# Optimization experiments

Hardware: AMD Instinct MI355X
Metric: run time of the kernel (lower is better)

## Reference

```python
import jax, jax.numpy as jnp
import numpy as np

D_MODEL = 2048
N_HEADS = 16
N_KV = 4
GROUP = N_HEADS // N_KV  # 4
D_K = D_MODEL // N_HEADS  # 128
D_V = D_MODEL // N_KV     # 512
THETA = 10000.0
Q_DIM = N_HEADS * D_K
K_DIM = N_KV * D_K
V_DIM = N_KV * D_V


def _apply_rope(t, sin, cos):
    # t: [B, H, L, D]; sin/cos: [L, D] broadcast over batch/heads
    half = t.shape[-1] // 2
    x1, x2 = t[..., :half], t[..., half:]
    rot = jnp.concatenate([-x2, x1], axis=-1)
    return t * cos + rot * sin


def setup_inputs() -> dict:
    key = jax.random.key(0)
    k1, k2, k3 = jax.random.split(key, 3)
    x = jax.random.normal(k1, (2, 2048, D_MODEL), dtype=jnp.float32)
    # attn_proj: Linear(d_model -> Q_DIM+K_DIM+V_DIM, bias=False); stored as [in, out]
    W_attn = jax.random.normal(k2, (D_MODEL, Q_DIM + K_DIM + V_DIM), dtype=jnp.float32) * 0.02
    # out_proj: Linear(n_heads*d_v -> d_model) with bias
    W_out = jax.random.normal(k3, (N_HEADS * D_V, D_MODEL), dtype=jnp.float32) * 0.02
    b_out = jnp.zeros((D_MODEL,), dtype=jnp.float32)
    return {"x": x, "W_attn": W_attn, "W_out": W_out, "b_out": b_out}


def reference(x, W_attn, W_out, b_out):
    B, L, _ = x.shape
    qkv = x @ W_attn  # [B, L, Q_DIM+K_DIM+V_DIM]
    q = qkv[..., :Q_DIM].reshape(B, L, N_HEADS, D_K).transpose(0, 2, 1, 3)          # [B,H,L,dk]
    k = qkv[..., Q_DIM:Q_DIM + K_DIM].reshape(B, L, N_KV, D_K).transpose(0, 2, 1, 3)  # [B,Hkv,L,dk]
    v = qkv[..., Q_DIM + K_DIM:].reshape(B, L, N_KV, D_V).transpose(0, 2, 1, 3)       # [B,Hkv,L,dv]

    # RoPE (computed in float32, as in source)
    inv_freq = 1.0 / (THETA ** (jnp.arange(0, D_K, 2, dtype=jnp.float32) / D_K))
    freqs = jnp.arange(L, dtype=jnp.float32)[:, None] * inv_freq[None, :]  # [L, dk/2]
    ang = jnp.concatenate([freqs, freqs], axis=-1)                          # [L, dk]
    sin, cos = jnp.sin(ang), jnp.cos(ang)
    q = _apply_rope(q.astype(jnp.float32), sin, cos).astype(x.dtype)
    k = _apply_rope(k.astype(jnp.float32), sin, cos).astype(x.dtype)

    # GQA: repeat_interleave(group, dim=1) is equivalent to grouping q heads as [kv, group]
    qg = q.reshape(B, N_KV, GROUP, L, D_K)
    scores = jnp.einsum('bkgqd,bkld->bkgql', qg, k) / (D_K ** 0.5)  # [B,Hkv,G,L,L]
    probs = jax.nn.softmax(scores, axis=-1)
    ctx = jnp.einsum('bkgql,bkle->bkgqe', probs, v)  # [B,Hkv,G,L,dv]
    ctx = ctx.reshape(B, N_HEADS, L, D_V).transpose(0, 2, 1, 3).reshape(B, L, N_HEADS * D_V)
    return ctx @ W_out + b_out
```

## Files before the change

kernel.cpp:

```cpp
#include <hip/hip_runtime.h>

typedef unsigned short u16;
typedef float f32x4 __attribute__((ext_vector_type(4)));
typedef __bf16 bf16x8 __attribute__((ext_vector_type(8)));

#define DEV static __device__ __forceinline__

DEV u16 f2bf(float f) {
  union { float f; unsigned u; } c; c.f = f;
  unsigned u = c.u;
  u += 0x7fffu + ((u >> 16) & 1u);
  return (u16)(u >> 16);
}
DEV float bf2f(u16 h) {
  union { float f; unsigned u; } c; c.u = ((unsigned)h) << 16;
  return c.f;
}
DEV f32x4 MFMA(bf16x8 a, bf16x8 b, f32x4 c) {
  return __builtin_amdgcn_mfma_f32_16x16x32_bf16(a, b, c, 0, 0, 0);
}
DEV unsigned cvt_pk_bf16(float a, float b) {
  unsigned r;
  asm("v_cvt_pk_bf16_f32 %0, %1, %2" : "=v"(r) : "v"(a), "v"(b));
  return r;
}
DEV float ex2(float x) { return __builtin_amdgcn_exp2f(x); }
DEV void glds16(const void* src, void* lds) {
  __builtin_amdgcn_global_load_lds(
      (__attribute__((address_space(1))) void*)src,
      (__attribute__((address_space(3))) void*)lds, 16, 0, 0);
}
DEV void barrier_raw() {
  __builtin_amdgcn_sched_barrier(0);
  asm volatile("s_barrier" ::: "memory");
  __builtin_amdgcn_sched_barrier(0);
}
#define VMCNT(N)                                              \
  do {                                                        \
    asm volatile("s_waitcnt vmcnt(" #N ")" ::: "memory");     \
    __builtin_amdgcn_sched_barrier(0);                        \
  } while (0)


__global__ void rope_tables(float* __restrict__ sinT, float* __restrict__ cosT) {
  int idx = blockIdx.x * 256 + threadIdx.x;
  int l = idx >> 6, i = idx & 63;
  float inv = __expf(-((float)(2 * i) / 128.0f) * 9.210340371976184f);
  float ang = (float)l * inv;
  sinT[idx] = sinf(ang);
  cosT[idx] = cosf(ang);
}

__global__ void cast_f32_bf16(const float* __restrict__ in, u16* __restrict__ out) {
  int i = (blockIdx.x * 256 + threadIdx.x) * 4;
  float4 v = *(const float4*)(in + i);
  ushort4 o;
  o.x = f2bf(v.x); o.y = f2bf(v.y); o.z = f2bf(v.z); o.w = f2bf(v.w);
  *(ushort4*)(out + i) = o;
}

__global__ void transpose_cast(const float* __restrict__ in, u16* __restrict__ out,
                               int R, int C) {
  __shared__ u16 tile[32][33];
  int c0 = blockIdx.x * 32, r0 = blockIdx.y * 32;
  int tx = threadIdx.x, ty = threadIdx.y;
  for (int i = 0; i < 32; i += 8)
    tile[ty + i][tx] = f2bf(in[(size_t)(r0 + ty + i) * C + c0 + tx]);
  __syncthreads();
  for (int i = 0; i < 32; i += 8)
    out[(size_t)(c0 + ty + i) * R + r0 + tx] = tile[tx][ty + i];
}

__global__ __launch_bounds__(512) void gemm1_8ph(const u16* __restrict__ A,
                                                 const u16* __restrict__ Bt,
                                                 u16* __restrict__ C) {
  constexpr int K = 2048, N = 4608, NT = 32;
  __shared__ __align__(16) u16 lA[2][2][8192];
  __shared__ __align__(16) u16 lB[2][2][8192];
  const int t = threadIdx.x, w = t >> 6, l = t & 63;
  const int lr = l & 15, lg = l >> 4;
  const int wr = w >> 2, wn = w & 3;
  const int swz = (blockIdx.x & 7) * 36 + (blockIdx.x >> 3);
  const int bm = swz & 15, bn = swz >> 4;

  const size_t aBase = (size_t)(bm * 256) * K;
  const size_t bBase = (size_t)(bn * 256) * K;
  const int lslog = (t & 3) ^ ((t >> 3) & 3);
  const int r128 = t >> 2;
  const int aswz = (lg ^ ((lr >> 1) & 3)) << 4;

  auto stA = [&](int buf, int kk, int tile) {
#pragma unroll
    for (int i = 0; i < 2; ++i) {
      int row = i * 128 + r128;
      glds16(A + aBase + (size_t)row * K + tile * 64 + kk * 32 + lslog * 8,
             &lA[buf][kk][i * 4096 + t * 8]);
    }
  };
  auto stB = [&](int buf, int kk, int tile) {
#pragma unroll
    for (int i = 0; i < 2; ++i) {
      int row = i * 128 + r128;
      glds16(Bt + bBase + (size_t)row * K + tile * 64 + kk * 32 + lslog * 8,
             &lB[buf][kk][i * 4096 + t * 8]);
    }
  };

  f32x4 acc[8][4];
#pragma unroll
  for (int f = 0; f < 8; ++f)
#pragma unroll
    for (int g = 0; g < 4; ++g) acc[f][g] = f32x4{0.f, 0.f, 0.f, 0.f};

  stA(0, 0, 0); stB(0, 0, 0); stA(0, 1, 0); stB(0, 1, 0); stA(1, 0, 1); stB(1, 0, 1);
  VMCNT(8);
  barrier_raw();

  auto PH = [&](int buf, int kk, int mh, auto&& st) {
    bf16x8 af[4], bb[4];
    const char* pA = (const char*)lA[buf][kk];
    const char* pB = (const char*)lB[buf][kk];
#pragma unroll
    for (int f = 0; f < 4; ++f) {
      af[f] = *(const bf16x8*)(pA + (wr * 128 + (mh * 4 + f) * 16 + lr) * 64 + aswz);
      bb[f] = *(const bf16x8*)(pB + (wn * 64 + f * 16 + lr) * 64 + aswz);
    }
    st();
    __builtin_amdgcn_s_setprio(1);
#pragma unroll
    for (int f = 0; f < 4; ++f)
#pragma unroll
      for (int g = 0; g < 4; ++g)
        acc[mh * 4 + f][g] = MFMA(af[f], bb[g], acc[mh * 4 + f][g]);
    __builtin_amdgcn_s_setprio(0);
  };
  auto NOST = [] {};

  for (int i = 0; i < NT / 2 - 1; ++i) {
    const int t1 = 2 * i + 1, t2 = 2 * i + 2, t3 = 2 * i + 3;
    PH(0, 0, 0, [&] { stA(1, 1, t1); });            barrier_raw();
    PH(0, 0, 1, [&] { stB(1, 1, t1); }); VMCNT(8);  barrier_raw();
    PH(0, 1, 0, [&] { stA(0, 0, t2); });            barrier_raw();
    PH(0, 1, 1, [&] { stB(0, 0, t2); }); VMCNT(8);  barrier_raw();
    PH(1, 0, 0, [&] { stA(0, 1, t2); });            barrier_raw();
    PH(1, 0, 1, [&] { stB(0, 1, t2); }); VMCNT(8);  barrier_raw();
    PH(1, 1, 0, [&] { stA(1, 0, t3); });            barrier_raw();
    PH(1, 1, 1, [&] { stB(1, 0, t3); }); VMCNT(8);  barrier_raw();
  }
  PH(0, 0, 0, [&] { stA(1, 1, NT - 1); });           barrier_raw();
  PH(0, 0, 1, [&] { stB(1, 1, NT - 1); }); VMCNT(8); barrier_raw();
  PH(0, 1, 0, NOST);                                 barrier_raw();
  PH(0, 1, 1, NOST);                       VMCNT(4); barrier_raw();
  PH(1, 0, 0, NOST);                                 barrier_raw();
  PH(1, 0, 1, NOST);                       VMCNT(0); barrier_raw();
  PH(1, 1, 0, NOST);                                 barrier_raw();
  PH(1, 1, 1, NOST);

  const int crow0 = bm * 256 + wr * 128;
  const int ccol0 = bn * 256 + wn * 64;
#pragma unroll
  for (int f = 0; f < 8; ++f)
#pragma unroll
    for (int g = 0; g < 4; ++g)
#pragma unroll
      for (int j = 0; j < 4; ++j)
        C[(size_t)(crow0 + f * 16 + lg * 4 + j) * N + ccol0 + g * 16 + lr] =
            f2bf(acc[f][g][j]);
}

__global__ __launch_bounds__(512) void gemm2_4ph(const u16* __restrict__ A,
                                                 const u16* __restrict__ Bt,
                                                 float* __restrict__ Cf,
                                                 const float* __restrict__ bias) {
  constexpr int K = 8192, N = 2048, NT = 128;
  __shared__ __align__(16) u16 lA[2][2][8192];
  __shared__ __align__(16) u16 lB[2][2][4096];
  const int t = threadIdx.x, w = t >> 6, l = t & 63;
  const int lr = l & 15, lg = l >> 4;
  const int wr = w >> 1, wn = w & 1;
  const int swz = (blockIdx.x & 7) * 32 + (blockIdx.x >> 3);
  const int bm = swz & 15, bn = swz >> 4;

  const size_t aBase = (size_t)(bm * 256) * K;
  const size_t bBase = (size_t)(bn * 128) * K;
  const int lslog = (t & 3) ^ ((t >> 3) & 3);
  const int r128 = t >> 2;
  const int aswz = (lg ^ ((lr >> 1) & 3)) << 4;

  auto stA = [&](int buf, int kk, int tile) {
#pragma unroll
    for (int i = 0; i < 2; ++i) {
      int row = i * 128 + r128;
      glds16(A + aBase + (size_t)row * K + tile * 64 + kk * 32 + lslog * 8,
             &lA[buf][kk][i * 4096 + t * 8]);
    }
  };
  auto stB = [&](int buf, int kk, int tile) {
    glds16(Bt + bBase + (size_t)r128 * K + tile * 64 + kk * 32 + lslog * 8,
           &lB[buf][kk][t * 8]);
  };

  f32x4 acc[4][4];
#pragma unroll
  for (int f = 0; f < 4; ++f)
#pragma unroll
    for (int g = 0; g < 4; ++g) acc[f][g] = f32x4{0.f, 0.f, 0.f, 0.f};

  stA(0, 0, 0); stB(0, 0, 0); stA(0, 1, 0); stB(0, 1, 0); stA(1, 0, 1); stB(1, 0, 1);
  VMCNT(6);
  barrier_raw();

  auto PH = [&](int buf, int kk, auto&& st) {
    bf16x8 af[4], bb[4];
    const char* pA = (const char*)lA[buf][kk];
    const char* pB = (const char*)lB[buf][kk];
#pragma unroll
    for (int f = 0; f < 4; ++f) {
      af[f] = *(const bf16x8*)(pA + (wr * 64 + f * 16 + lr) * 64 + aswz);
      bb[f] = *(const bf16x8*)(pB + (wn * 64 + f * 16 + lr) * 64 + aswz);
    }
    st();
    __builtin_amdgcn_s_setprio(1);
#pragma unroll
    for (int f = 0; f < 4; ++f)
#pragma unroll
      for (int g = 0; g < 4; ++g)
        acc[f][g] = MFMA(af[f], bb[g], acc[f][g]);
    __builtin_amdgcn_s_setprio(0);
  };
  auto NOST = [] {};

  for (int i = 0; i < NT / 2 - 1; ++i) {
    const int t1 = 2 * i + 1, t2 = 2 * i + 2, t3 = 2 * i + 3;
    PH(0, 0, [&] { stA(1, 1, t1); stB(1, 1, t1); }); VMCNT(6); barrier_raw();
    PH(0, 1, [&] { stA(0, 0, t2); stB(0, 0, t2); }); VMCNT(6); barrier_raw();
    PH(1, 0, [&] { stA(0, 1, t2); stB(0, 1, t2); }); VMCNT(6); barrier_raw();
    PH(1, 1, [&] { stA(1, 0, t3); stB(1, 0, t3); }); VMCNT(6); barrier_raw();
  }
  PH(0, 0, [&] { stA(1, 1, NT - 1); stB(1, 1, NT - 1); }); VMCNT(6); barrier_raw();
  PH(0, 1, NOST);                                          VMCNT(3); barrier_raw();
  PH(1, 0, NOST);                                          VMCNT(0); barrier_raw();
  PH(1, 1, NOST);

  const int crow0 = bm * 256 + wr * 64;
  const int ccol0 = bn * 128 + wn * 64;
#pragma unroll
  for (int g = 0; g < 4; ++g) {
    float bv = bias[ccol0 + g * 16 + lr];
#pragma unroll
    for (int f = 0; f < 4; ++f)
#pragma unroll
      for (int j = 0; j < 4; ++j)
        Cf[(size_t)(crow0 + f * 16 + lg * 4 + j) * N + ccol0 + g * 16 + lr] =
            acc[f][g][j] + bv;
  }
}

__global__ void rope_kernel(u16* __restrict__ qkv, const float* __restrict__ sinT,
                            const float* __restrict__ cosT) {
  int idx = blockIdx.x * 256 + threadIdx.x;
  int d = idx & 63;
  int rh = idx >> 6;
  int head = rh % 20;
  int row = rh / 20;
  int lpos = row & 2047;
  int col = head < 16 ? head * 128 : 2048 + (head - 16) * 128;
  float sc = head < 16 ? 0.12751743561938476f : 1.0f;
  u16* p = qkv + (size_t)row * 4608 + col;
  float x1 = bf2f(p[d]), x2 = bf2f(p[d + 64]);
  float c = cosT[lpos * 64 + d], s = sinT[lpos * 64 + d];
  p[d]      = f2bf((x1 * c - x2 * s) * sc);
  p[d + 64] = f2bf((x2 * c + x1 * s) * sc);
}

__global__ void vt_kernel(const u16* __restrict__ qkv, u16* __restrict__ vT) {
  __shared__ u16 tile[32][33];
  int bkv = blockIdx.z;
  int b = bkv >> 2, kv = bkv & 3;
  int e0 = blockIdx.x * 32, l0 = blockIdx.y * 32;
  const u16* src = qkv + (size_t)(b * 2048) * 4608 + 2560 + kv * 512;
  int tx = threadIdx.x, ty = threadIdx.y;
  for (int i = 0; i < 32; i += 8)
    tile[ty + i][tx] = src[(size_t)(l0 + ty + i) * 4608 + e0 + tx];
  __syncthreads();
  u16* dst = vT + (size_t)(bkv * 512) * 2048;
  int pi = ((tx >> 2) & 3) * 8 + ((tx >> 4) & 1) * 4 + (tx & 3);
  for (int i = 0; i < 32; i += 8)
    dst[(size_t)(e0 + ty + i) * 2048 + l0 + pi] = tile[tx][ty + i];
}

__global__ __launch_bounds__(512, 2) void attn_kernel(
    const u16* __restrict__ qkv, const u16* __restrict__ vT,
    u16* __restrict__ ctxb) {
  const int wg = blockIdx.x;
  const int pg = wg & 7, qt = wg >> 3;
  const int kvg = pg & 3, b = pg >> 2;
  const int t = threadIdx.x, w = t >> 6, l = t & 63;
  const int lr = l & 15, lg = l >> 4;
  const int h4 = w >> 1, eh = w & 1;
  const int h = kvg * 4 + h4;

  __shared__ __align__(16) u16 lK[2][32 * 128];
  __shared__ __align__(16) u16 lV[2][256 * 64];

  f32x4 zero = {0.f, 0.f, 0.f, 0.f};

  bf16x8 qf[2][4];
  const size_t qbase = (size_t)(b * 2048 + qt * 32);
#pragma unroll
  for (int m = 0; m < 2; ++m)
#pragma unroll
    for (int dc = 0; dc < 4; ++dc)
      qf[m][dc] = *(const bf16x8*)(qkv + (qbase + m * 16 + lr) * 4608 + h * 128 + dc * 32 + lg * 8);

  f32x4 acc[2][16];
#pragma unroll
  for (int m = 0; m < 2; ++m)
#pragma unroll
    for (int e = 0; e < 16; ++e) acc[m][e] = zero;
  float m_r[2] = {-1e30f, -1e30f};
  float l_r[2] = {0.f, 0.f};

  const size_t kbase = (size_t)(b * 2048) * 4608 + 2048 + kvg * 128;
  const size_t vbase = (size_t)((b * 4 + kvg) * 512) * 2048;

  const int krow = t >> 4;
  const int kp = t & 15;
  const int ks = (kp & 8) | ((kp ^ (krow & 7)) & 7);
  const u16* ksrc0 = qkv + kbase + (size_t)krow * 4608 + ks * 8;
  const int vs = (t & 7) ^ ((t >> 3) & 7);
  const int ve0 = (t >> 3) * 2 + (vs >> 2);
  const u16* vsrc0 = vT + vbase + (size_t)ve0 * 2048 + (vs & 3) * 8;

  const int vfoff = (eh * 128 + (lr >> 1)) * 128 +
                    (((((lr & 1) << 2) | lg) ^ ((lr >> 1) & 7)) << 4);

  auto stage = [&](int bi, int kv0) {
    glds16(ksrc0 + (size_t)kv0 * 4608, &lK[bi][t * 8]);
#pragma unroll
    for (int i = 0; i < 4; ++i)
      glds16(vsrc0 + kv0 + (size_t)i * 262144, &lV[bi][i * 4096 + t * 8]);
  };

  stage(0, 0);

  for (int it = 0; it < 64; ++it) {
    const int cur = it & 1;
    __syncthreads();
    if (it + 1 < 64) stage(cur ^ 1, 32 * (it + 1));
    const char* lKc = (const char*)lK[cur];
    const char* lVc = (const char*)lV[cur];

    f32x4 sT[2][2];
    sT[0][0] = zero; sT[0][1] = zero; sT[1][0] = zero; sT[1][1] = zero;
#pragma unroll
    for (int dc = 0; dc < 4; ++dc) {
      int slot = dc * 4 + lg;
      int sw = (slot & 8) | ((slot ^ (lr & 7)) & 7);
#pragma unroll
      for (int kt = 0; kt < 2; ++kt) {
        bf16x8 kf = *(const bf16x8*)(lKc + (kt * 16 + lr) * 256 + sw * 16);
        sT[kt][0] = MFMA(kf, qf[0][dc], sT[kt][0]);
        sT[kt][1] = MFMA(kf, qf[1][dc], sT[kt][1]);
      }
    }

    float rmax[2];
#pragma unroll
    for (int m = 0; m < 2; ++m) {
      float a0 = fmaxf(fmaxf(sT[0][m][0], sT[0][m][1]), fmaxf(sT[0][m][2], sT[0][m][3]));
      float a1 = fmaxf(fmaxf(sT[1][m][0], sT[1][m][1]), fmaxf(sT[1][m][2], sT[1][m][3]));
      float r = fmaxf(a0, a1);
      r = fmaxf(r, __shfl_xor(r, 16));
      r = fmaxf(r, __shfl_xor(r, 32));
      rmax[m] = r;
    }
    bool need = (rmax[0] > m_r[0] + 11.5f) || (rmax[1] > m_r[1] + 11.5f);
    if (__any(need)) {
#pragma unroll
      for (int m = 0; m < 2; ++m) {
        float mn = fmaxf(m_r[m], rmax[m]);
        float al = ex2(m_r[m] - mn);
        m_r[m] = mn; l_r[m] *= al;
        float alj[4];
#pragma unroll
        for (int j = 0; j < 4; ++j) alj[j] = __shfl(al, lg * 4 + j);
#pragma unroll
        for (int e = 0; e < 16; ++e)
#pragma unroll
          for (int j = 0; j < 4; ++j) acc[m][e][j] *= alj[j];
      }
    }

    bf16x8 pf[2];
#pragma unroll
    for (int m = 0; m < 2; ++m) {
      float p0 = ex2(sT[0][m][0] - m_r[m]), p1 = ex2(sT[0][m][1] - m_r[m]);
      float p2 = ex2(sT[0][m][2] - m_r[m]), p3 = ex2(sT[0][m][3] - m_r[m]);
      float p4 = ex2(sT[1][m][0] - m_r[m]), p5 = ex2(sT[1][m][1] - m_r[m]);
      float p6 = ex2(sT[1][m][2] - m_r[m]), p7 = ex2(sT[1][m][3] - m_r[m]);
      float s = ((p0 + p1) + (p2 + p3)) + ((p4 + p5) + (p6 + p7));
      s += __shfl_xor(s, 16);
      s += __shfl_xor(s, 32);
      l_r[m] += s;
      union { bf16x8 v; unsigned wd[4]; } u;
      u.wd[0] = cvt_pk_bf16(p0, p1);
      u.wd[1] = cvt_pk_bf16(p2, p3);
      u.wd[2] = cvt_pk_bf16(p4, p5);
      u.wd[3] = cvt_pk_bf16(p6, p7);
      pf[m] = u.v;
    }

#pragma unroll
    for (int e = 0; e < 16; ++e) {
      bf16x8 vf = *(const bf16x8*)(lVc + vfoff + e * 1024);
      acc[0][e] = MFMA(pf[0], vf, acc[0][e]);
      acc[1][e] = MFMA(pf[1], vf, acc[1][e]);
    }
  }

#pragma unroll
  for (int m = 0; m < 2; ++m) {
    float linv[4];
#pragma unroll
    for (int j = 0; j < 4; ++j) linv[j] = 1.0f / __shfl(l_r[m], lg * 4 + j);
    const size_t orow0 = qbase + m * 16 + lg * 4;
#pragma unroll
    for (int e = 0; e < 16; ++e)
#pragma unroll
      for (int j = 0; j < 4; ++j)
        ctxb[(orow0 + j) * 8192 + h * 512 + eh * 256 + e * 16 + lr] =
            f2bf(acc[m][e][j] * linv[j]);
  }
}

extern "C" void kernel_launch(void* const* d_in, const int* in_sizes, int n_in,
                              void* d_out, int out_size, void* d_ws, size_t ws_size,
                              hipStream_t stream) {
  const float* x      = (const float*)d_in[0];
  const float* W_attn = (const float*)d_in[1];
  const float* W_out  = (const float*)d_in[2];
  const float* b_out  = (const float*)d_in[3];
  float* out = (float*)d_out;
  char* ws = (char*)d_ws;

  if (ws_size < 158334976u) return;

  float* sinT = (float*)(ws + 0);
  float* cosT = (float*)(ws + 524288);
  u16* xb   = (u16*)(ws + 1048576);
  u16* WbT  = (u16*)(ws + 17825792);
  u16* qkvb = (u16*)(ws + 36700160);
  u16* vT   = (u16*)(ws + 74448896);
  u16* ctxb = (u16*)(ws + 91226112);
  u16* WobT = (u16*)(ws + 1048576);

  rope_tables<<<512, 256, 0, stream>>>(sinT, cosT);
  cast_f32_bf16<<<8192, 256, 0, stream>>>(x, xb);
  transpose_cast<<<dim3(144, 64), dim3(32, 8), 0, stream>>>(W_attn, WbT, 2048, 4608);
  gemm1_8ph<<<288, 512, 0, stream>>>(xb, WbT, qkvb);
  rope_kernel<<<20480, 256, 0, stream>>>(qkvb, sinT, cosT);
  vt_kernel<<<dim3(16, 64, 8), dim3(32, 8), 0, stream>>>(qkvb, vT);
  attn_kernel<<<512, 512, 0, stream>>>(qkvb, vT, ctxb);
  transpose_cast<<<dim3(64, 256), dim3(32, 8), 0, stream>>>(W_out, WobT, 8192, 2048);
  gemm2_4ph<<<256, 512, 0, stream>>>(ctxb, WobT, out, b_out);
}
```

Baseline: 571.6 us.

## Software-pipeline PV matmul one iteration behind QK with triple-buffered V

Restructures the attention loop so the P·V MFMAs for the previous tile run interleaved with the exp computations of the current tile, using a triple-buffered V LDS ring so the previous tile's V stays resident. When a max-rescale is needed, the pending PV is flushed before rescaling. It also adds s_setprio around the MFMA sections. The aim is to overlap transcendental/VALU work with matrix work. In exchange, LDS use grows by one 32 KB V buffer, which may reduce occupancy below 2 workgroups per CU, and register pressure rises.

```diff
diff --git a/kernel.cpp b/kernel.cpp
--- a/kernel.cpp
+++ b/kernel.cpp
@@ -301,7 +301,7 @@
   const int h = kvg * 4 + h4;
 
   __shared__ __align__(16) u16 lK[2][32 * 128];
-  __shared__ __align__(16) u16 lV[2][256 * 64];
+  __shared__ __align__(16) u16 lV[3][256 * 64];
 
   f32x4 zero = {0.f, 0.f, 0.f, 0.f};
 
@@ -335,24 +335,32 @@
   const int vfoff = (eh * 128 + (lr >> 1)) * 128 +
                     (((((lr & 1) << 2) | lg) ^ ((lr >> 1) & 7)) << 4);
 
-  auto stage = [&](int bi, int kv0) {
-    glds16(ksrc0 + (size_t)kv0 * 4608, &lK[bi][t * 8]);
+  auto stageK = [&](int kb, int kv0) {
+    glds16(ksrc0 + (size_t)kv0 * 4608, &lK[kb][t * 8]);
+  };
+  auto stageV = [&](u16* vbuf, int kv0) {
 #pragma unroll
     for (int i = 0; i < 4; ++i)
-      glds16(vsrc0 + kv0 + (size_t)i * 262144, &lV[bi][i * 4096 + t * 8]);
-  };
-
-  stage(0, 0);
+      glds16(vsrc0 + kv0 + (size_t)i * 262144, vbuf + i * 4096 + t * 8);
+  };
+
+  u16* vP = lV[2];
+  u16* vC = lV[0];
+  u16* vS = lV[1];
+
+  stageK(0, 0); stageV(vC, 0);
+
+  bf16x8 pfp[2];
 
   for (int it = 0; it < 64; ++it) {
-    const int cur = it & 1;
     __syncthreads();
-    if (it + 1 < 64) stage(cur ^ 1, 32 * (it + 1));
-    const char* lKc = (const char*)lK[cur];
-    const char* lVc = (const char*)lV[cur];
+    if (it + 1 < 64) { stageK((it + 1) & 1, 32 * (it + 1)); stageV(vS, 32 * (it + 1)); }
+    const char* lKc = (const char*)lK[it & 1];
+    const char* vPc = (const char*)vP;
 
     f32x4 sT[2][2];
     sT[0][0] = zero; sT[0][1] = zero; sT[1][0] = zero; sT[1][1] = zero;
+    __builtin_amdgcn_s_setprio(1);
 #pragma unroll
     for (int dc = 0; dc < 4; ++dc) {
       int slot = dc * 4 + lg;
@@ -364,6 +372,20 @@
         sT[kt][1] = MFMA(kf, qf[1][dc], sT[kt][1]);
       }
     }
+    __builtin_amdgcn_s_setprio(0);
+
+    auto PVC = [&](int c) {
+      if (it) {
+        __builtin_amdgcn_s_setprio(1);
+#pragma unroll
+        for (int e = c * 4; e < c * 4 + 4; ++e) {
+          bf16x8 vf = *(const bf16x8*)(vPc + vfoff + e * 1024);
+          acc[0][e] = MFMA(pfp[0], vf, acc[0][e]);
+          acc[1][e] = MFMA(pfp[1], vf, acc[1][e]);
+        }
+        __builtin_amdgcn_s_setprio(0);
+      }
+    };
 
     float rmax[2];
 #pragma unroll
@@ -376,7 +398,9 @@
       rmax[m] = r;
     }
     bool need = (rmax[0] > m_r[0] + 11.5f) || (rmax[1] > m_r[1] + 11.5f);
+
     if (__any(need)) {
+      PVC(0); PVC(1); PVC(2); PVC(3);
 #pragma unroll
       for (int m = 0; m < 2; ++m) {
         float mn = fmaxf(m_r[m], rmax[m]);
@@ -390,35 +414,56 @@
 #pragma unroll
           for (int j = 0; j < 4; ++j) acc[m][e][j] *= alj[j];
       }
-    }
-
-    bf16x8 pf[2];
+#pragma unroll
+      for (int m = 0; m < 2; ++m)
+#pragma unroll
+        for (int kt = 0; kt < 2; ++kt)
+#pragma unroll
+          for (int j = 0; j < 4; ++j) sT[kt][m][j] = ex2(sT[kt][m][j] - m_r[m]);
+    } else {
+#pragma unroll
+      for (int j = 0; j < 4; ++j) sT[0][0][j] = ex2(sT[0][0][j] - m_r[0]);
+      PVC(0);
+#pragma unroll
+      for (int j = 0; j < 4; ++j) sT[1][0][j] = ex2(sT[1][0][j] - m_r[0]);
+      PVC(1);
+#pragma unroll
+      for (int j = 0; j < 4; ++j) sT[0][1][j] = ex2(sT[0][1][j] - m_r[1]);
+      PVC(2);
+#pragma unroll
+      for (int j = 0; j < 4; ++j) sT[1][1][j] = ex2(sT[1][1][j] - m_r[1]);
+      PVC(3);
+    }
+
 #pragma unroll
     for (int m = 0; m < 2; ++m) {
-      float p0 = ex2(sT[0][m][0] - m_r[m]), p1 = ex2(sT[0][m][1] - m_r[m]);
-      float p2 = ex2(sT[0][m][2] - m_r[m]), p3 = ex2(sT[0][m][3] - m_r[m]);
-      float p4 = ex2(sT[1][m][0] - m_r[m]), p5 = ex2(sT[1][m][1] - m_r[m]);
-      float p6 = ex2(sT[1][m][2] - m_r[m]), p7 = ex2(sT[1][m][3] - m_r[m]);
-      float s = ((p0 + p1) + (p2 + p3)) + ((p4 + p5) + (p6 + p7));
+      float s = ((sT[0][m][0] + sT[0][m][1]) + (sT[0][m][2] + sT[0][m][3])) +
+                ((sT[1][m][0] + sT[1][m][1]) + (sT[1][m][2] + sT[1][m][3]));
       s += __shfl_xor(s, 16);
       s += __shfl_xor(s, 32);
       l_r[m] += s;
       union { bf16x8 v; unsigned wd[4]; } u;
-      u.wd[0] = cvt_pk_bf16(p0, p1);
-      u.wd[1] = cvt_pk_bf16(p2, p3);
-      u.wd[2] = cvt_pk_bf16(p4, p5);
-      u.wd[3] = cvt_pk_bf16(p6, p7);
-      pf[m] = u.v;
-    }
-
+      u.wd[0] = cvt_pk_bf16(sT[0][m][0], sT[0][m][1]);
+      u.wd[1] = cvt_pk_bf16(sT[0][m][2], sT[0][m][3]);
+      u.wd[2] = cvt_pk_bf16(sT[1][m][0], sT[1][m][1]);
+      u.wd[3] = cvt_pk_bf16(sT[1][m][2], sT[1][m][3]);
+      pfp[m] = u.v;
+    }
+
+    u16* tmp = vP; vP = vC; vC = vS; vS = tmp;
+  }
+
+  {
+    const char* vPc = (const char*)vP;
+    __builtin_amdgcn_s_setprio(1);
 #pragma unroll
     for (int e = 0; e < 16; ++e) {
-      bf16x8 vf = *(const bf16x8*)(lVc + vfoff + e * 1024);
-      acc[0][e] = MFMA(pf[0], vf, acc[0][e]);
-      acc[1][e] = MFMA(pf[1], vf, acc[1][e]);
-    }
+      bf16x8 vf = *(const bf16x8*)(vPc + vfoff + e * 1024);
+      acc[0][e] = MFMA(pfp[0], vf, acc[0][e]);
+      acc[1][e] = MFMA(pfp[1], vf, acc[1][e]);
+    }
+    __builtin_amdgcn_s_setprio(0);
   }
-
 #pragma unroll
   for (int m = 0; m < 2; ++m) {
     float linv[4];
```

Result: slower. 1.982 ms (+246.7%).
